# Kernel optimization log

Hardware: AMD Instinct MI355X
Metric: run time of the kernel (lower is better)

The kernel has to match this reference:

```python
import jax, jax.numpy as jnp
import numpy as np

BUCKET_BINS = np.array([0, 1, 2, 3, 4, 5, 7, 8, 15, 16, 31, 32, 63, 64], dtype=np.int32)
MAX_WINDOW = 8  # args.span_maximum_length


def _span_index_table(L):
    # Static enumeration of all spans of width 1..MAX_WINDOW (stride-1 unfold).
    starts, ends = [], []
    for w in range(1, min(L, MAX_WINDOW) + 1):
        s = np.arange(0, L - w + 1)
        starts.append(s)
        ends.append(s + w)
    return (np.concatenate(starts).astype(np.int32),
            np.concatenate(ends).astype(np.int32))


def _bucket(width):
    # index of last bin with width >= bin value
    return jnp.searchsorted(jnp.asarray(BUCKET_BINS), width, side='right') - 1


def _fnn(h, W1, b1, W2, b2, W3, b3):
    # Linear->ReLU->(Dropout: eval identity)->Linear->ReLU->Linear->Softmax
    h = jax.nn.relu(h @ W1 + b1)
    h = jax.nn.relu(h @ W2 + b2)
    return jax.nn.softmax(h @ W3 + b3, axis=-1)


def setup_inputs() -> dict:
    key = jax.random.key(0)
    ks = jax.random.split(key, 16)
    B, L, D = 8, 256, 768
    H, WD, DD = 1024, 25, 25
    span_dim = 2 * D + WD          # 1561
    pair_dim = 2 * span_dim + DD   # 3147
    f = jnp.float32

    def g(k, shape, scale):
        return jax.random.normal(k, shape, dtype=f) * scale

    return {
        'x': g(ks[0], (B, L, D), 1.0),
        'width_emb': g(ks[1], (len(BUCKET_BINS), WD), 0.02),
        'dist_emb': g(ks[2], (len(BUCKET_BINS), DD), 0.02),
        'Ws1': g(ks[3], (span_dim, H), 0.02), 'bs1': jnp.zeros((H,), f),
        'Ws2': g(ks[4], (H, H), 0.02), 'bs2': jnp.zeros((H,), f),
        'Ws3': g(ks[5], (H, 3), 0.02), 'bs3': jnp.zeros((3,), f),
        'Wp1': g(ks[6], (pair_dim, H), 0.02), 'bp1': jnp.zeros((H,), f),
        'Wp2': g(ks[7], (H, H), 0.02), 'bp2': jnp.zeros((H,), f),
        'Wp3': g(ks[8], (H, 4), 0.02), 'bp3': jnp.zeros((4,), f),
        'nz': 64,
    }


def reference(x, width_emb, dist_emb, Ws1, bs1, Ws2, bs2, Ws3, bs3,
              Wp1, bp1, Wp2, bp2, Wp3, bp3, nz):
    B, L, D = x.shape
    starts_np, ends_np = _span_index_table(L)
    starts = jnp.asarray(starts_np)
    ends = jnp.asarray(ends_np)

    # ---- SpanRepresentation: [start token, end token, width bucket emb] ----
    w_emb = width_emb[_bucket(ends - starts)]                     # [S, WD]
    spans = jnp.concatenate([
        x[:, starts_np, :],                                       # [B,S,D]
        x[:, ends_np - 1, :],                                     # [B,S,D]
        jnp.broadcast_to(w_emb, (B,) + w_emb.shape),              # [B,S,WD]
    ], axis=-1)                                                   # [B,S,span_dim]

    # ---- span_fnn + PrunedTargetOpinion (top-k on aspect/opinion probs) ----
    span_prob = _fnn(spans, Ws1, bs1, Ws2, bs2, Ws3, bs3)         # [B,S,3]
    _, t_idx = jax.lax.top_k(span_prob[:, :, 1], nz)              # aspect  [B,nz]
    _, o_idx = jax.lax.top_k(span_prob[:, :, 2], nz)              # opinion [B,nz]

    # ---- PairRepresentation: all target x opinion pairs ----
    t_rep = jnp.take_along_axis(spans, t_idx[:, :, None], axis=1) # [B,nz,sd]
    o_rep = jnp.take_along_axis(spans, o_idx[:, :, None], axis=1)
    ta, tb = starts[t_idx], ends[t_idx]                           # [B,nz]
    oc, od = starts[o_idx], ends[o_idx]
    # min_distance(a,b,c,d) = min(|b-c|, |a-d|)
    dist = jnp.minimum(jnp.abs(tb[:, :, None] - oc[:, None, :]),
                       jnp.abs(ta[:, :, None] - od[:, None, :]))  # [B,nz,nz]
    d_emb = dist_emb[_bucket(dist)]                               # [B,nz,nz,DD]
    sd = spans.shape[-1]
    pairs = jnp.concatenate([
        jnp.broadcast_to(t_rep[:, :, None, :], (B, nz, nz, sd)),
        jnp.broadcast_to(o_rep[:, None, :, :], (B, nz, nz, sd)),
        d_emb,
    ], axis=-1).reshape(B, nz * nz, 2 * sd + d_emb.shape[-1])     # [B,nz^2,pair_dim]

    pair_prob = _fnn(pairs, Wp1, bp1, Wp2, bp2, Wp3, bp3)         # [B,nz^2,4]
    return span_prob, pair_prob
```

## Files before the change

kernel.cpp:

```cpp
#include <hip/hip_runtime.h>
#include <cstdint>
#include <cstddef>

#define BATCH 8
#define SEQ   256
#define DIM   768
#define NSPAN 2020
#define HID   1024
#define NZ    64

typedef unsigned short u16;
typedef unsigned int   u32;
typedef unsigned long long u64;

typedef __bf16 bf16x8 __attribute__((ext_vector_type(8)));
typedef float  f32x4  __attribute__((ext_vector_type(4)));

__device__ __forceinline__ u16 f2bf(float f) {
    union { float f; u32 u; } x; x.f = f;
    u32 r = x.u + 0x7fffu + ((x.u >> 16) & 1u);
    return (u16)(r >> 16);
}
__device__ __forceinline__ float bf2f(u16 b) {
    union { u32 u; float f; } x; x.u = ((u32)b) << 16;
    return x.f;
}
__device__ __forceinline__ void splitbf(float v, u16& h, u16& l) {
    h = f2bf(v);
    l = f2bf(v - bf2f(h));
}

__device__ __forceinline__ void gld_lds16(const void* g, void* l) {
    __builtin_amdgcn_global_load_lds(
        (const __attribute__((address_space(1))) unsigned int*)g,
        (__attribute__((address_space(3))) unsigned int*)l, 16, 0, 0);
}

__device__ __forceinline__ void span_decode(int s, int& start, int& end, int& w) {
    int off = 0;
#pragma unroll
    for (int wi = 1; wi <= 8; ++wi) {
        int cnt = SEQ - wi + 1;
        if (s < off + cnt) { w = wi; start = s - off; end = start + wi; return; }
        off += cnt;
    }
    w = 8; start = 0; end = 8;
}

__device__ __forceinline__ int dbucket(int d) {
    int b = 0;
    b += (d >= 1);  b += (d >= 2);  b += (d >= 3);  b += (d >= 4);
    b += (d >= 5);  b += (d >= 7);  b += (d >= 8);  b += (d >= 15);
    b += (d >= 16); b += (d >= 31); b += (d >= 32); b += (d >= 63);
    b += (d >= 64);
    return b;
}

__device__ __forceinline__ void xcd_map(int L, int sft, int& bx, int& by) {
    int grp = L >> (3 + sft);
    int rem = L & ((1 << (3 + sft)) - 1);
    bx = rem >> 3;
    by = (grp << 3) | (rem & 7);
}

__global__ __launch_bounds__(256) void k_prep(
    const float* __restrict__ x,  u16* __restrict__ xh,   u16* __restrict__ xl,
    const float* __restrict__ wemb, const float* __restrict__ demb,
    const float* __restrict__ bs1, const float* __restrict__ bp1,
    float* __restrict__ wtabS, float* __restrict__ wtabPt,
    float* __restrict__ wtabPo, float* __restrict__ dtab,
    const float* __restrict__ Ws1, u16* __restrict__ W1Th, u16* __restrict__ W1Tl,
    const float* __restrict__ Ws2, u16* __restrict__ W2Th, u16* __restrict__ W2Tl,
    const float* __restrict__ Wp2, u16* __restrict__ Wp2T,
    const float* __restrict__ Wp1, u16* __restrict__ Wp1T4)
{
    __shared__ float tile[32][33];
    const int bid = blockIdx.x, tid = threadIdx.x;
    if (bid < 6144) {
        int i = bid * 256 + tid;
        u16 h, l; splitbf(x[i], h, l);
        xh[i] = h; xl[i] = l;
        return;
    }
    if (bid < 6296) {
        int t = bid - 6144;
        int row = t >> 2;
        int h = (t & 3) * 256 + tid;
        const int wb[8] = {1,2,3,4,5,5,6,7};
        if (row < 8) {
            int bk = wb[row];
            float acc = bs1[h];
            for (int j = 0; j < 25; ++j) acc = fmaf(wemb[bk*25+j], Ws1[(size_t)(1536+j)*HID + h], acc);
            wtabS[row*HID + h] = acc;
        } else if (row < 16) {
            int bk = wb[row-8];
            float acc = 0.f;
            for (int j = 0; j < 25; ++j) acc = fmaf(wemb[bk*25+j], Wp1[(size_t)(1536+j)*HID + h], acc);
            wtabPt[(row-8)*HID + h] = acc;
        } else if (row < 24) {
            int bk = wb[row-16];
            float acc = 0.f;
            for (int j = 0; j < 25; ++j) acc = fmaf(wemb[bk*25+j], Wp1[(size_t)(3097+j)*HID + h], acc);
            wtabPo[(row-16)*HID + h] = acc;
        } else {
            int tt = row - 24;
            float acc = bp1[h];
            for (int j = 0; j < 25; ++j) acc = fmaf(demb[tt*25+j], Wp1[(size_t)(3122+j)*HID + h], acc);
            dtab[tt*HID + h] = acc;
        }
        return;
    }
    const int tb = bid - 6296;
    const int tr = tid >> 3;
    const int tc4 = (tid & 7) * 4;
    int job, tk, tn, blk = 0;
    if (tb < 1536)      { job = 0; tk = tb % 24; tn = tb / 24; }
    else if (tb < 2560) { job = 1; int t = tb - 1536; tk = t & 31; tn = t >> 5; }
    else if (tb < 3584) { job = 2; int t = tb - 2560; tk = t & 31; tn = t >> 5; }
    else                { job = 3; int t = tb - 3584; blk = t / 768; int r = t - blk * 768; tk = r % 24; tn = r / 24; }
    const int k0 = tk * 32, n0 = tn * 32;

    int k = k0 + tr;
    float4 v;
    if (job == 0) {
        const float* s = (n0 < 1024) ? (Ws1 + (size_t)k * HID + n0)
                                     : (Ws1 + (size_t)(768 + k) * HID + (n0 - 1024));
        v = *(const float4*)(s + tc4);
    } else if (job == 1) {
        v = *(const float4*)(Ws2 + (size_t)k * HID + n0 + tc4);
    } else if (job == 2) {
        v = *(const float4*)(Wp2 + (size_t)k * HID + n0 + tc4);
    } else {
        const int roff[4] = {0, 768, 1561, 2329};
        v = *(const float4*)(Wp1 + (size_t)(roff[blk] + k) * HID + n0 + tc4);
    }
    tile[tr][tc4+0] = v.x; tile[tr][tc4+1] = v.y;
    tile[tr][tc4+2] = v.z; tile[tr][tc4+3] = v.w;
    __syncthreads();

    int nn = n0 + tr;
    float w0 = tile[tc4+0][tr], w1 = tile[tc4+1][tr];
    float w2 = tile[tc4+2][tr], w3 = tile[tc4+3][tr];
    if (job == 0) {
        size_t d = (size_t)nn * 768 + k0 + tc4;
        u16 h0,l0,h1,l1,h2,l2,h3,l3;
        splitbf(w0,h0,l0); splitbf(w1,h1,l1); splitbf(w2,h2,l2); splitbf(w3,h3,l3);
        *(uint2*)(W1Th + d) = make_uint2((u32)h0 | ((u32)h1 << 16), (u32)h2 | ((u32)h3 << 16));
        *(uint2*)(W1Tl + d) = make_uint2((u32)l0 | ((u32)l1 << 16), (u32)l2 | ((u32)l3 << 16));
    } else if (job == 1) {
        size_t d = (size_t)nn * 1024 + k0 + tc4;
        u16 h0,l0,h1,l1,h2,l2,h3,l3;
        splitbf(w0,h0,l0); splitbf(w1,h1,l1); splitbf(w2,h2,l2); splitbf(w3,h3,l3);
        *(uint2*)(W2Th + d) = make_uint2((u32)h0 | ((u32)h1 << 16), (u32)h2 | ((u32)h3 << 16));
        *(uint2*)(W2Tl + d) = make_uint2((u32)l0 | ((u32)l1 << 16), (u32)l2 | ((u32)l3 << 16));
    } else if (job == 2) {
        size_t d = (size_t)nn * 1024 + k0 + tc4;
        *(uint2*)(Wp2T + d) = make_uint2((u32)f2bf(w0) | ((u32)f2bf(w1) << 16),
                                         (u32)f2bf(w2) | ((u32)f2bf(w3) << 16));
    } else {
        size_t d = (size_t)blk * 786432 + (size_t)nn * 768 + k0 + tc4;
        *(uint2*)(Wp1T4 + d) = make_uint2((u32)f2bf(w0) | ((u32)f2bf(w1) << 16),
                                          (u32)f2bf(w2) | ((u32)f2bf(w3) << 16));
    }
}

__global__ __launch_bounds__(256) void k_gemm3bf(
    const u16* __restrict__ Ah, const u16* __restrict__ Al, int lda,
    const u16* __restrict__ BTh, const u16* __restrict__ BTl, int ldb,
    float* __restrict__ C, int ldc,
    int M, int K, int nby, int sft)
{
    int bx, by;
    xcd_map(blockIdx.x, sft, bx, by);
    if (by >= nby) return;
    __shared__ __align__(16) u16 sm[4 * 128 * 32];
    u16* sAh = sm;
    u16* sAl = sm + 4096;
    u16* sBh = sm + 8192;
    u16* sBl = sm + 12288;
    const int tid = threadIdx.x;
    const int bm = by * 128, bn = bx * 128;
    const int wave = tid >> 6, lane = tid & 63;
    const int wr = wave >> 1, wc = wave & 1;
    const int q = lane >> 4, tl = lane & 15;

    f32x4 zero = {0.f, 0.f, 0.f, 0.f};
    f32x4 acc[4][4];
#pragma unroll
    for (int i = 0; i < 4; ++i)
#pragma unroll
        for (int j = 0; j < 4; ++j) acc[i][j] = zero;

    const int srow = lane >> 2;
    const int scol = (lane & 3) * 8;
    int ra0 = bm + wave * 32 + srow;      if (ra0 >= M) ra0 = M - 1;
    int ra1 = bm + wave * 32 + 16 + srow; if (ra1 >= M) ra1 = M - 1;
    const int rb0 = bn + wave * 32 + srow;
    const int rb1 = bn + wave * 32 + 16 + srow;
    u16* dA0 = sAh + wave * 1024;  u16* dA1 = dA0 + 512;
    u16* dL0 = sAl + wave * 1024;  u16* dL1 = dL0 + 512;
    u16* dB0 = sBh + wave * 1024;  u16* dB1 = dB0 + 512;
    u16* dC0 = sBl + wave * 1024;  u16* dC1 = dC0 + 512;
    const u16* gA0 = Ah  + (size_t)ra0 * lda + scol;
    const u16* gA1 = Ah  + (size_t)ra1 * lda + scol;
    const u16* gL0 = Al  + (size_t)ra0 * lda + scol;
    const u16* gL1 = Al  + (size_t)ra1 * lda + scol;
    const u16* gB0 = BTh + (size_t)rb0 * ldb + scol;
    const u16* gB1 = BTh + (size_t)rb1 * ldb + scol;
    const u16* gC0 = BTl + (size_t)rb0 * ldb + scol;
    const u16* gC1 = BTl + (size_t)rb1 * ldb + scol;

    for (int k0 = 0; k0 < K; k0 += 32) {
        gld_lds16(gA0 + k0, dA0);
        gld_lds16(gA1 + k0, dA1);
        gld_lds16(gL0 + k0, dL0);
        gld_lds16(gL1 + k0, dL1);
        gld_lds16(gB0 + k0, dB0);
        gld_lds16(gB1 + k0, dB1);
        gld_lds16(gC0 + k0, dC0);
        gld_lds16(gC1 + k0, dC1);
        __syncthreads();
        bf16x8 ah[4], al[4], bh[4], bl[4];
#pragma unroll
        for (int t = 0; t < 4; ++t) {
            int arow = (wr*64 + t*16 + tl) * 32 + q*8;
            int brow = (wc*64 + t*16 + tl) * 32 + q*8;
            ah[t] = *(const bf16x8*)(&sAh[arow]);
            al[t] = *(const bf16x8*)(&sAl[arow]);
            bh[t] = *(const bf16x8*)(&sBh[brow]);
            bl[t] = *(const bf16x8*)(&sBl[brow]);
        }
#pragma unroll
        for (int ti = 0; ti < 4; ++ti)
#pragma unroll
            for (int tj = 0; tj < 4; ++tj) {
                acc[ti][tj] = __builtin_amdgcn_mfma_f32_16x16x32_bf16(ah[ti], bh[tj], acc[ti][tj], 0, 0, 0);
                acc[ti][tj] = __builtin_amdgcn_mfma_f32_16x16x32_bf16(al[ti], bh[tj], acc[ti][tj], 0, 0, 0);
                acc[ti][tj] = __builtin_amdgcn_mfma_f32_16x16x32_bf16(ah[ti], bl[tj], acc[ti][tj], 0, 0, 0);
            }
        __syncthreads();
    }
#pragma unroll
    for (int ti = 0; ti < 4; ++ti) {
#pragma unroll
        for (int tj = 0; tj < 4; ++tj) {
            int gcol = bn + wc*64 + tj*16 + tl;
#pragma unroll
            for (int r = 0; r < 4; ++r) {
                int grow = bm + wr*64 + ti*16 + q*4 + r;
                if (grow >= M) continue;
                C[(size_t)grow * ldc + gcol] = acc[ti][tj][r];
            }
        }
    }
}

#define MFB __builtin_amdgcn_mfma_f32_16x16x32_bf16
#define MFROW(i, A, B) \
    acc[i][0] = MFB(A, B[0], acc[i][0], 0, 0, 0); \
    acc[i][1] = MFB(A, B[1], acc[i][1], 0, 0, 0); \
    acc[i][2] = MFB(A, B[2], acc[i][2], 0, 0, 0); \
    acc[i][3] = MFB(A, B[3], acc[i][3], 0, 0, 0);

#define SPAN_PHASE(P, VMC, GLDS) \
    { \
        bf16x8 ah0 = *(const bf16x8*)(smr + rA + (2*(P)+0)*512); \
        bf16x8 ah1 = *(const bf16x8*)(smr + rA + (2*(P)+1)*512); \
        bf16x8 al0 = *(const bf16x8*)(smr + rA + 8192 + (2*(P)+0)*512); \
        bf16x8 al1 = *(const bf16x8*)(smr + rA + 8192 + (2*(P)+1)*512); \
        if ((P) == 0) { \
            bh[0] = *(const bf16x8*)(smr + rB + 0*512); \
            bh[1] = *(const bf16x8*)(smr + rB + 1*512); \
            bh[2] = *(const bf16x8*)(smr + rB + 2*512); \
            bh[3] = *(const bf16x8*)(smr + rB + 3*512); \
            bl[0] = *(const bf16x8*)(smr + rB + 8192 + 0*512); \
            bl[1] = *(const bf16x8*)(smr + rB + 8192 + 1*512); \
            bl[2] = *(const bf16x8*)(smr + rB + 8192 + 2*512); \
            bl[3] = *(const bf16x8*)(smr + rB + 8192 + 3*512); \
        } \
        GLDS \
        asm volatile("s_waitcnt vmcnt(" #VMC ")" ::: "memory"); \
        asm volatile("s_barrier" ::: "memory"); \
        __builtin_amdgcn_sched_barrier(0); \
        __builtin_amdgcn_s_setprio(1); \
        MFROW(2*(P)+0, ah0, bh) \
        MFROW(2*(P)+1, ah1, bh) \
        MFROW(2*(P)+0, al0, bh) \
        MFROW(2*(P)+1, al1, bh) \
        MFROW(2*(P)+0, ah0, bl) \
        MFROW(2*(P)+1, ah1, bl) \
        __builtin_amdgcn_s_setprio(0); \
        asm volatile("s_barrier" ::: "memory"); \
    }

__global__ __launch_bounds__(512, 2) void k_span_l2(
    const u16* __restrict__ Ah, const u16* __restrict__ Al,
    const u16* __restrict__ BTh, const u16* __restrict__ BTl,
    const float* __restrict__ bs2, const float* __restrict__ Ws3,
    float* __restrict__ part, int M)
{
    __shared__ __align__(16) u16 sm[65536];
    const int tid = threadIdx.x;
    const int swz = (blockIdx.x & 7) * 32 + (blockIdx.x >> 3);
    const int by = swz >> 2, bx = swz & 3;
    const int bm = by * 256, bn = bx * 256;
    const int wave = tid >> 6, lane = tid & 63;
    const int wm = wave >> 2, wn = wave & 3;
    const int tl = lane & 15, q8 = lane >> 4;

    const int sr  = lane >> 2;
    const int scs = lane & 3;
    const int scl = scs ^ ((sr >> 1) & 3);
    const u16* gsrc[8];
    u32 ldst[8];
#pragma unroll
    for (int c = 0; c < 4; ++c) {
        int arr  = 2 + (c >> 1);
        int half = c & 1;
        int sb   = wave;
        int row  = bn + half * 128 + sb * 16 + sr;
        const u16* base = (arr == 2) ? BTh : BTl;
        gsrc[c] = base + (size_t)row * HID + scl * 8;
        ldst[c] = arr * 8192 + half * 4096 + sb * 512;
    }
#pragma unroll
    for (int p = 0; p < 4; ++p) {
        int arr  = wave >> 2;
        int half = (wave >> 1) & 1;
        int sb   = 2 * p + (wave & 1);
        int row  = bm + half * 128 + sb * 16 + sr;
        if (row >= M) row = M - 1;
        const u16* base = arr ? Al : Ah;
        gsrc[4 + p] = base + (size_t)row * HID + scl * 8;
        ldst[4 + p] = arr * 8192 + half * 4096 + sb * 512;
    }
    const int cpr = q8 ^ ((tl >> 1) & 3);
    const u32 lof = (u32)(tl * 32 + cpr * 8);
    const u32 rA  = (u32)(wm * 4096) + lof;
    const u32 rB  = 16384u + (u32)((wn >> 1) * 4096 + (wn & 1) * 2048) + lof;

    f32x4 zero = {0.f, 0.f, 0.f, 0.f};
    f32x4 acc[8][4];
#pragma unroll
    for (int i = 0; i < 8; ++i)
#pragma unroll
        for (int j = 0; j < 4; ++j) acc[i][j] = zero;

#pragma unroll
    for (int c = 0; c < 8; ++c) gld_lds16(gsrc[c], sm + ldst[c]);
    asm volatile("s_waitcnt vmcnt(3)" ::: "memory");
    asm volatile("s_barrier" ::: "memory");

    bf16x8 bh[4], bl[4];
    for (int t = 0; t < 32; ++t) {
        const u16* smr = sm + ((t & 1) ? 32768u : 0u);
        u16*       smw = sm + ((t & 1) ? 0u : 32768u);
        const int  kn  = (t + 1) * 32;
        SPAN_PHASE(0, 5,
            gld_lds16(gsrc[0] + kn, smw + ldst[0]);
            gld_lds16(gsrc[1] + kn, smw + ldst[1]);
            gld_lds16(gsrc[2] + kn, smw + ldst[2]);)
        SPAN_PHASE(1, 6,
            gld_lds16(gsrc[3] + kn, smw + ldst[3]);
            gld_lds16(gsrc[4] + kn, smw + ldst[4]);)
        SPAN_PHASE(2, 7,
            gld_lds16(gsrc[5] + kn, smw + ldst[5]);
            gld_lds16(gsrc[6] + kn, smw + ldst[6]);)
        SPAN_PHASE(3, 3,
            gld_lds16(gsrc[7] + kn, smw + ldst[7]);)
    }

    const int slot = bx * 4 + wn;
#pragma unroll
    for (int fm = 0; fm < 8; ++fm) {
#pragma unroll
        for (int r = 0; r < 4; ++r) {
            int grow = bm + wm * 128 + fm * 16 + q8 * 4 + r;
            float l0 = 0.f, l1 = 0.f, l2 = 0.f;
#pragma unroll
            for (int fn = 0; fn < 4; ++fn) {
                int gcol = bn + wn * 64 + fn * 16 + tl;
                float v = fmaxf(acc[fm][fn][r] + bs2[gcol], 0.f);
                const float* w3 = Ws3 + gcol * 3;
                l0 = fmaf(v, w3[0], l0);
                l1 = fmaf(v, w3[1], l1);
                l2 = fmaf(v, w3[2], l2);
            }
#pragma unroll
            for (int off = 8; off > 0; off >>= 1) {
                l0 += __shfl_down(l0, off, 16);
                l1 += __shfl_down(l1, off, 16);
                l2 += __shfl_down(l2, off, 16);
            }
            if (tl == 0 && grow < M) {
                float* dst = part + ((size_t)grow * 16 + slot) * 3;
                dst[0] = l0; dst[1] = l1; dst[2] = l2;
            }
        }
    }
    asm volatile("s_waitcnt vmcnt(0)" ::: "memory");
}

__global__ __launch_bounds__(256) void k_pairL1(
    const u16* __restrict__ xh, const u16* __restrict__ Wp1T4,
    float* __restrict__ TO2, const int* __restrict__ toks)
{
    __shared__ __align__(16) u16 sm[2 * 64 * 32];
    u16* sA = sm;
    u16* sB = sm + 2048;
    const int tid = threadIdx.x;
    const int bid = blockIdx.x;
    const int p = bid >> 8;
    const int bx = bid & 15, by = (bid >> 4) & 15;
    const int bm = by * 64, bn = bx * 64;
    const int wave = tid >> 6, lane = tid & 63;
    const int wr = wave >> 1, wc = wave & 1;
    const int q = lane >> 4, tl = lane & 15;
    const bool isO = bm >= 512;

    f32x4 zero = {0.f, 0.f, 0.f, 0.f};
    f32x4 acc[2][2];
#pragma unroll
    for (int i = 0; i < 2; ++i)
#pragma unroll
        for (int j = 0; j < 2; ++j) acc[i][j] = zero;

    const int srow = tid >> 2;
    const int scol = (tid & 3) * 8;
    u16* dA = sA + wave * 512;
    u16* dB = sB + wave * 512;

    int arow = toks[bm + srow + p * 1024];
    const u16* gA = xh + (size_t)arow * DIM + scol;
    const u16* gB = Wp1T4 + ((size_t)((isO ? 2 : 0) + p) * 1024 + bn + srow) * DIM + scol;
    for (int k0 = 0; k0 < DIM; k0 += 32) {
        gld_lds16(gA + k0, dA);
        gld_lds16(gB + k0, dB);
        __syncthreads();
        bf16x8 af[2], bf[2];
#pragma unroll
        for (int t = 0; t < 2; ++t) {
            af[t] = *(const bf16x8*)(&sA[(wr*32 + t*16 + tl) * 32 + q*8]);
            bf[t] = *(const bf16x8*)(&sB[(wc*32 + t*16 + tl) * 32 + q*8]);
        }
#pragma unroll
        for (int ti = 0; ti < 2; ++ti)
#pragma unroll
            for (int tj = 0; tj < 2; ++tj)
                acc[ti][tj] = __builtin_amdgcn_mfma_f32_16x16x32_bf16(af[ti], bf[tj], acc[ti][tj], 0, 0, 0);
        __syncthreads();
    }
    float* dstb = TO2 + (size_t)p * 1024 * HID;
#pragma unroll
    for (int ti = 0; ti < 2; ++ti) {
#pragma unroll
        for (int tj = 0; tj < 2; ++tj) {
            int gcol = bn + wc*32 + tj*16 + tl;
#pragma unroll
            for (int r = 0; r < 4; ++r) {
                int grow = bm + wr*32 + ti*16 + q*4 + r;
                dstb[(size_t)grow * HID + gcol] = acc[ti][tj][r];
            }
        }
    }
}

__global__ __launch_bounds__(256) void k_build_h1s(
    const float* __restrict__ XALL, const float* __restrict__ wtabS,
    u16* __restrict__ h1h, u16* __restrict__ h1l)
{
    int r = blockIdx.x;
    int b = r / NSPAN, s = r - b * NSPAN;
    int st, en, w; span_decode(s, st, en, w);
    const float4* xs = (const float4*)(XALL + (size_t)(b*SEQ + st) * 2048);
    const float4* xe = (const float4*)(XALL + (size_t)(b*SEQ + en - 1) * 2048 + 1024);
    const float4* wt = (const float4*)(wtabS + (size_t)(w-1) * HID);
    int t = threadIdx.x;
    float4 a = xs[t], bz = xe[t], c = wt[t];
    float v0 = fmaxf(a.x + bz.x + c.x, 0.f);
    float v1 = fmaxf(a.y + bz.y + c.y, 0.f);
    float v2 = fmaxf(a.z + bz.z + c.z, 0.f);
    float v3 = fmaxf(a.w + bz.w + c.w, 0.f);
    u16 h0,l0,h1,l1,h2,l2,h3,l3;
    splitbf(v0,h0,l0); splitbf(v1,h1,l1); splitbf(v2,h2,l2); splitbf(v3,h3,l3);
    size_t base = (size_t)r * HID + t * 4;
    *(uint2*)(h1h + base) = make_uint2((u32)h0 | ((u32)h1 << 16), (u32)h2 | ((u32)h3 << 16));
    *(uint2*)(h1l + base) = make_uint2((u32)l0 | ((u32)l1 << 16), (u32)l2 | ((u32)l3 << 16));
}

__global__ __launch_bounds__(1024) void k_topk(
    const float* __restrict__ partS, const float* __restrict__ bs3,
    float* __restrict__ out, int* __restrict__ t_idx, int* __restrict__ o_idx,
    int* __restrict__ toks)
{
    int b = blockIdx.x >> 1;
    int head = 1 + (blockIdx.x & 1);
    int* outp = (head == 1 ? t_idx : o_idx) + b * NZ;
    __shared__ u64 keys[2048];
    int tid = threadIdx.x;
#pragma unroll
    for (int ii = 0; ii < 2; ++ii) {
        int s = tid + ii * 1024;
        u32 fb = 0;
        if (s < NSPAN) {
            const float* p = partS + (size_t)(b * NSPAN + s) * 48;
            float s0 = bs3[0], s1 = bs3[1], s2 = bs3[2];
#pragma unroll
            for (int t = 0; t < 16; ++t) {
                s0 += p[t*3]; s1 += p[t*3+1]; s2 += p[t*3+2];
            }
            float m = fmaxf(s0, fmaxf(s1, s2));
            float e0 = expf(s0 - m), e1 = expf(s1 - m), e2 = expf(s2 - m);
            float inv = 1.f / (e0 + e1 + e2);
            float p0 = e0 * inv, p1 = e1 * inv, p2 = e2 * inv;
            float* o = out + (size_t)(b * NSPAN + s) * 3;
            o[0] = p0; o[1] = p1; o[2] = p2;
            union { float f; u32 u; } x;
            x.f = (head == 1) ? p1 : p2;
            fb = x.u;
        }
        keys[s] = ((u64)fb << 32) | (u64)(0xFFFFFFFFu - (u32)s);
    }
    __syncthreads();
    for (int k = 2; k <= 2048; k <<= 1) {
        for (int j = k >> 1; j > 0; j >>= 1) {
#pragma unroll
            for (int ii = 0; ii < 2; ++ii) {
                int i = tid + ii * 1024;
                int ixj = i ^ j;
                if (ixj > i) {
                    u64 a = keys[i], c = keys[ixj];
                    bool desc = (i & k) == 0;
                    bool wrong = desc ? (a < c) : (a > c);
                    if (wrong) { keys[i] = c; keys[ixj] = a; }
                }
            }
            __syncthreads();
        }
    }
    if (tid < NZ) {
        u64 key = keys[tid];
        int fi = (int)(0xFFFFFFFFu - (u32)(key & 0xFFFFFFFFu));
        if (fi < 0 || fi >= NSPAN) fi = 0;
        outp[tid] = fi;
        int st, en, w; span_decode(fi, st, en, w);
        int base = (head == 1 ? 0 : 512) + b * NZ + tid;
        toks[base] = b * SEQ + st;
        toks[1024 + base] = b * SEQ + en - 1;
    }
}

__global__ __launch_bounds__(256) void k_build_h1p(
    const float* __restrict__ TO2, const int* __restrict__ t_idx, const int* __restrict__ o_idx,
    const float* __restrict__ wtabPt, const float* __restrict__ wtabPo,
    const float* __restrict__ dtab, u16* __restrict__ h1p)
{
    __shared__ float Ts[8][HID];
    __shared__ float Os[4][HID];
    const int bid = blockIdx.x;
    const int b = bid >> 7;
    const int it = (bid >> 4) & 7;
    const int jt = bid & 15;
    const int i0 = it * 8, j0 = jt * 4;
    const int tid = threadIdx.x;
    const int k4 = tid * 4;
    const size_t PS = (size_t)1024 * HID;

    int tinfo[8][2];
    int oinfo[4][2];
#pragma unroll
    for (int r = 0; r < 8; ++r) {
        int i = i0 + r;
        int ts = t_idx[b*64 + i];
        int ta, tb, wt; span_decode(ts, ta, tb, wt);
        tinfo[r][0] = ta; tinfo[r][1] = tb;
        float4 t0 = *(const float4*)(TO2 + (size_t)(b*64 + i) * HID + k4);
        float4 t1 = *(const float4*)(TO2 + PS + (size_t)(b*64 + i) * HID + k4);
        float4 pp = *(const float4*)(wtabPt + (size_t)(wt-1) * HID + k4);
        Ts[r][k4+0] = t0.x + t1.x + pp.x;
        Ts[r][k4+1] = t0.y + t1.y + pp.y;
        Ts[r][k4+2] = t0.z + t1.z + pp.z;
        Ts[r][k4+3] = t0.w + t1.w + pp.w;
    }
#pragma unroll
    for (int r = 0; r < 4; ++r) {
        int j = j0 + r;
        int os = o_idx[b*64 + j];
        int oc, od, wo; span_decode(os, oc, od, wo);
        oinfo[r][0] = oc; oinfo[r][1] = od;
        float4 o0 = *(const float4*)(TO2 + (size_t)(512 + b*64 + j) * HID + k4);
        float4 o1 = *(const float4*)(TO2 + PS + (size_t)(512 + b*64 + j) * HID + k4);
        float4 qq = *(const float4*)(wtabPo + (size_t)(wo-1) * HID + k4);
        Os[r][k4+0] = o0.x + o1.x + qq.x;
        Os[r][k4+1] = o0.y + o1.y + qq.y;
        Os[r][k4+2] = o0.z + o1.z + qq.z;
        Os[r][k4+3] = o0.w + o1.w + qq.w;
    }
    __syncthreads();

#pragma unroll
    for (int ri = 0; ri < 8; ++ri) {
#pragma unroll
        for (int rj = 0; rj < 4; ++rj) {
            int ta = tinfo[ri][0], tb = tinfo[ri][1];
            int oc = oinfo[rj][0], od = oinfo[rj][1];
            int d1 = tb - oc; d1 = d1 < 0 ? -d1 : d1;
            int d2 = ta - od; d2 = d2 < 0 ? -d2 : d2;
            int dist = d1 < d2 ? d1 : d2;
            int db = dbucket(dist);
            const float4 dd = *(const float4*)(dtab + (size_t)db * HID + k4);
            float vx = fmaxf(Ts[ri][k4+0] + Os[rj][k4+0] + dd.x, 0.f);
            float vy = fmaxf(Ts[ri][k4+1] + Os[rj][k4+1] + dd.y, 0.f);
            float vz = fmaxf(Ts[ri][k4+2] + Os[rj][k4+2] + dd.z, 0.f);
            float vw = fmaxf(Ts[ri][k4+3] + Os[rj][k4+3] + dd.w, 0.f);
            u32 p0 = (u32)f2bf(vx) | ((u32)f2bf(vy) << 16);
            u32 p1 = (u32)f2bf(vz) | ((u32)f2bf(vw) << 16);
            int row = b * 4096 + (i0 + ri) * 64 + (j0 + rj);
            *(uint2*)(h1p + (size_t)row * HID + k4) = make_uint2(p0, p1);
        }
    }
}

#define PAIR_PHASE(P, VMC, GLDS) \
    { \
        bf16x8 a00 = *(const bf16x8*)(smr + rA + ((2*(P)+0)*2+0)*512); \
        bf16x8 a01 = *(const bf16x8*)(smr + rA + ((2*(P)+0)*2+1)*512); \
        bf16x8 a10 = *(const bf16x8*)(smr + rA + ((2*(P)+1)*2+0)*512); \
        bf16x8 a11 = *(const bf16x8*)(smr + rA + ((2*(P)+1)*2+1)*512); \
        if ((P) == 0) { \
            b0[0] = *(const bf16x8*)(smr + rB + 0*512); \
            b1[0] = *(const bf16x8*)(smr + rB + 1*512); \
            b0[1] = *(const bf16x8*)(smr + rB + 2*512); \
            b1[1] = *(const bf16x8*)(smr + rB + 3*512); \
            b0[2] = *(const bf16x8*)(smr + rB + 4*512); \
            b1[2] = *(const bf16x8*)(smr + rB + 5*512); \
            b0[3] = *(const bf16x8*)(smr + rB + 6*512); \
            b1[3] = *(const bf16x8*)(smr + rB + 7*512); \
        } \
        GLDS \
        asm volatile("s_waitcnt vmcnt(" #VMC ")" ::: "memory"); \
        asm volatile("s_barrier" ::: "memory"); \
        __builtin_amdgcn_sched_barrier(0); \
        __builtin_amdgcn_s_setprio(1); \
        MFROW(2*(P)+0, a00, b0) \
        MFROW(2*(P)+1, a10, b0) \
        MFROW(2*(P)+0, a01, b1) \
        MFROW(2*(P)+1, a11, b1) \
        __builtin_amdgcn_s_setprio(0); \
        asm volatile("s_barrier" ::: "memory"); \
    }

__global__ __launch_bounds__(512, 2) void k_pair_l2(
    const u16* __restrict__ Abf, const u16* __restrict__ BT,
    const float* __restrict__ bp2, const float* __restrict__ Wp3,
    float* __restrict__ part)
{
    __shared__ __align__(16) u16 sm[65536];
    const int tid = threadIdx.x;
    const int swz = (blockIdx.x & 7) * 64 + (blockIdx.x >> 3);
    const int by = swz >> 2, bx = swz & 3;
    const int bm = by * 256, bn = bx * 256;
    const int wave = tid >> 6, lane = tid & 63;
    const int wm = wave >> 2, wn = wave & 3;
    const int tl = lane & 15, q8 = lane >> 4;

    const int sr  = lane >> 2;
    const int scs = lane & 3;
    const int scl = scs ^ ((sr >> 1) & 3);
    const u16* gsrc[8];
    u32 ldst[8];
#pragma unroll
    for (int c = 0; c < 4; ++c) {
        int half = c >> 1;
        int sb   = (c & 1) * 8 + wave;
        int row  = bn + half * 128 + (sb >> 1) * 16 + sr;
        gsrc[c] = BT + (size_t)row * HID + (sb & 1) * 32 + scl * 8;
        ldst[c] = 16384 + half * 8192 + sb * 512;
    }
#pragma unroll
    for (int p = 0; p < 4; ++p) {
        int half = wave >> 2;
        int sb   = 4 * p + (wave & 3);
        int row  = bm + half * 128 + (sb >> 1) * 16 + sr;
        gsrc[4 + p] = Abf + (size_t)row * HID + (sb & 1) * 32 + scl * 8;
        ldst[4 + p] = half * 8192 + sb * 512;
    }
    const int cpr = q8 ^ ((tl >> 1) & 3);
    const u32 lof = (u32)(tl * 32 + cpr * 8);
    const u32 rA  = (u32)(wm * 8192) + lof;
    const u32 rB  = 16384u + (u32)((wn >> 1) * 8192 + (wn & 1) * 4096) + lof;

    f32x4 zero = {0.f, 0.f, 0.f, 0.f};
    f32x4 acc[8][4];
#pragma unroll
    for (int i = 0; i < 8; ++i)
#pragma unroll
        for (int j = 0; j < 4; ++j) acc[i][j] = zero;

#pragma unroll
    for (int c = 0; c < 8; ++c) gld_lds16(gsrc[c], sm + ldst[c]);
    asm volatile("s_waitcnt vmcnt(3)" ::: "memory");
    asm volatile("s_barrier" ::: "memory");

    bf16x8 b0[4], b1[4];
    for (int t = 0; t < 16; ++t) {
        const u16* smr = sm + ((t & 1) ? 32768u : 0u);
        u16*       smw = sm + ((t & 1) ? 0u : 32768u);
        const int  kn  = (t + 1) * 64;
        PAIR_PHASE(0, 5,
            gld_lds16(gsrc[0] + kn, smw + ldst[0]);
            gld_lds16(gsrc[1] + kn, smw + ldst[1]);
            gld_lds16(gsrc[2] + kn, smw + ldst[2]);)
        PAIR_PHASE(1, 6,
            gld_lds16(gsrc[3] + kn, smw + ldst[3]);
            gld_lds16(gsrc[4] + kn, smw + ldst[4]);)
        PAIR_PHASE(2, 7,
            gld_lds16(gsrc[5] + kn, smw + ldst[5]);
            gld_lds16(gsrc[6] + kn, smw + ldst[6]);)
        PAIR_PHASE(3, 3,
            gld_lds16(gsrc[7] + kn, smw + ldst[7]);)
    }

    const int slot = bx * 4 + wn;
#pragma unroll
    for (int fm = 0; fm < 8; ++fm) {
#pragma unroll
        for (int r = 0; r < 4; ++r) {
            int grow = bm + wm * 128 + fm * 16 + q8 * 4 + r;
            float l0 = 0.f, l1 = 0.f, l2 = 0.f, l3 = 0.f;
#pragma unroll
            for (int fn = 0; fn < 4; ++fn) {
                int gcol = bn + wn * 64 + fn * 16 + tl;
                float v = fmaxf(acc[fm][fn][r] + bp2[gcol], 0.f);
                const float4 w = *(const float4*)(Wp3 + gcol * 4);
                l0 = fmaf(v, w.x, l0); l1 = fmaf(v, w.y, l1);
                l2 = fmaf(v, w.z, l2); l3 = fmaf(v, w.w, l3);
            }
#pragma unroll
            for (int off = 8; off > 0; off >>= 1) {
                l0 += __shfl_down(l0, off, 16);
                l1 += __shfl_down(l1, off, 16);
                l2 += __shfl_down(l2, off, 16);
                l3 += __shfl_down(l3, off, 16);
            }
            if (tl == 0) {
                float* dst = part + ((size_t)grow * 16 + slot) * 4;
                dst[0] = l0; dst[1] = l1; dst[2] = l2; dst[3] = l3;
            }
        }
    }
    asm volatile("s_waitcnt vmcnt(0)" ::: "memory");
}

__global__ __launch_bounds__(256) void k_pair_red(
    const float* __restrict__ part, const float* __restrict__ bp3,
    float* __restrict__ out)
{
    int r = blockIdx.x * 256 + threadIdx.x;
    const float4* p = (const float4*)(part + (size_t)r * 64);
    float s0 = bp3[0], s1 = bp3[1], s2 = bp3[2], s3 = bp3[3];
#pragma unroll
    for (int t = 0; t < 16; ++t) {
        float4 v = p[t];
        s0 += v.x; s1 += v.y; s2 += v.z; s3 += v.w;
    }
    float m = fmaxf(fmaxf(s0, s1), fmaxf(s2, s3));
    float e0 = expf(s0 - m), e1 = expf(s1 - m), e2 = expf(s2 - m), e3 = expf(s3 - m);
    float inv = 1.f / (e0 + e1 + e2 + e3);
    float* o = out + (size_t)r * 4;
    o[0] = e0 * inv; o[1] = e1 * inv; o[2] = e2 * inv; o[3] = e3 * inv;
}

extern "C" void kernel_launch(void* const* d_in, const int* in_sizes, int n_in,
                              void* d_out, int out_size, void* d_ws, size_t ws_size,
                              hipStream_t stream)
{
    const float* x    = (const float*)d_in[0];
    const float* wemb = (const float*)d_in[1];
    const float* demb = (const float*)d_in[2];
    const float* Ws1  = (const float*)d_in[3];
    const float* bs1  = (const float*)d_in[4];
    const float* Ws2  = (const float*)d_in[5];
    const float* bs2  = (const float*)d_in[6];
    const float* Ws3  = (const float*)d_in[7];
    const float* bs3  = (const float*)d_in[8];
    const float* Wp1  = (const float*)d_in[9];
    const float* bp1  = (const float*)d_in[10];
    const float* Wp2  = (const float*)d_in[11];
    const float* bp2  = (const float*)d_in[12];
    const float* Wp3  = (const float*)d_in[13];
    const float* bp3  = (const float*)d_in[14];
    float* out = (float*)d_out;
    char* ws = (char*)d_ws;

    const size_t RSZ = (size_t)32768 * HID * 2;
    size_t off = 0;
    auto alloc = [&](size_t bytes) -> void* {
        void* p = ws + off;
        off += (bytes + 255) & ~(size_t)255;
        return p;
    };
    char* R1 = (char*)alloc(RSZ);
    char* R2 = (char*)alloc(RSZ);
    u16*   h1h  = (u16*)R1;
    u16*   h1l  = (u16*)(R1 + (size_t)16160 * HID * 2);
    float* XALL = (float*)R2;
    u16*   xl   = (u16*)(R2 + (16u << 20));
    u16*   W1Th = (u16*)(R2 + (19u << 20));
    u16*   W1Tl = (u16*)(R2 + (22u << 20));
    u16*   h1p  = (u16*)R2;
    u16*   xh     = (u16*)alloc((size_t)2048 * DIM * 2);
    float* TO2    = (float*)alloc((size_t)2 * 1024 * HID * 4);
    float* partS  = (float*)alloc((size_t)16160 * 16 * 3 * 4);
    float* partP  = (float*)alloc((size_t)32768 * 16 * 4 * 4);
    u16*   W2Th   = (u16*)alloc((size_t)1024 * 1024 * 2);
    u16*   W2Tl   = (u16*)alloc((size_t)1024 * 1024 * 2);
    u16*   Wp2T   = (u16*)alloc((size_t)1024 * 1024 * 2);
    u16*   Wp1T4  = (u16*)alloc((size_t)4 * 1024 * 768 * 2);
    float* wtabS  = (float*)alloc(8 * HID * 4);
    float* wtabPt = (float*)alloc(8 * HID * 4);
    float* wtabPo = (float*)alloc(8 * HID * 4);
    float* dtab   = (float*)alloc(14 * HID * 4);
    int*   t_idx  = (int*)alloc(BATCH * NZ * 4);
    int*   o_idx  = (int*)alloc(BATCH * NZ * 4);
    int*   toks   = (int*)alloc(2048 * 4);
    (void)ws_size; (void)in_sizes; (void)n_in; (void)out_size;

    k_prep<<<12952, 256, 0, stream>>>(x, xh, xl, wemb, demb, bs1, bp1,
                                      wtabS, wtabPt, wtabPo, dtab,
                                      Ws1, W1Th, W1Tl, Ws2, W2Th, W2Tl,
                                      Wp2, Wp2T, Wp1, Wp1T4);

    k_gemm3bf<<<256, 256, 0, stream>>>(xh, xl, 768, W1Th, W1Tl, 768,
                                       XALL, 2048, 2048, 768, 16, 4);
    k_build_h1s<<<16160, 256, 0, stream>>>(XALL, wtabS, h1h, h1l);
    k_span_l2<<<256, 512, 0, stream>>>(h1h, h1l, W2Th, W2Tl, bs2, Ws3, partS, 16160);
    k_topk<<<16, 1024, 0, stream>>>(partS, bs3, out, t_idx, o_idx, toks);
    k_pairL1<<<512, 256, 0, stream>>>(xh, Wp1T4, TO2, toks);
    k_build_h1p<<<1024, 256, 0, stream>>>(TO2, t_idx, o_idx, wtabPt, wtabPo, dtab, h1p);
    k_pair_l2<<<512, 512, 0, stream>>>(h1p, Wp2T, bp2, Wp3, partP);
    k_pair_red<<<128, 256, 0, stream>>>(partP, bp3, out + 48480);
}
```

Baseline: 410.5 us.

## Software-pipeline LDS fragment reads into registers in span and pair GEMM loops

Restructures the main K loops of the span and pair layer-2 GEMM kernels. The A fragments for the next phase are double-buffered in two register sets (X/Y), and the B fragments for the next tile are loaded at the end of each iteration. This lets the LDS reads overlap the MFMA work of the current phase and drops the trailing barrier after each phase. The risk is that the end-of-iteration reads from the write buffer may run before all async global-to-LDS copies have landed, since only vmcnt(3) is waited on. The change also raises register pressure.

New measurement: 410.5 us. No clear change (-0.0%).

```diff
diff --git a/kernel.cpp b/kernel.cpp
--- a/kernel.cpp
+++ b/kernel.cpp
@@ -262,37 +262,6 @@
     acc[i][2] = MFB(A, B[2], acc[i][2], 0, 0, 0); \
     acc[i][3] = MFB(A, B[3], acc[i][3], 0, 0, 0);
 
-#define SPAN_PHASE(P, VMC, GLDS) \
-    { \
-        bf16x8 ah0 = *(const bf16x8*)(smr + rA + (2*(P)+0)*512); \
-        bf16x8 ah1 = *(const bf16x8*)(smr + rA + (2*(P)+1)*512); \
-        bf16x8 al0 = *(const bf16x8*)(smr + rA + 8192 + (2*(P)+0)*512); \
-        bf16x8 al1 = *(const bf16x8*)(smr + rA + 8192 + (2*(P)+1)*512); \
-        if ((P) == 0) { \
-            bh[0] = *(const bf16x8*)(smr + rB + 0*512); \
-            bh[1] = *(const bf16x8*)(smr + rB + 1*512); \
-            bh[2] = *(const bf16x8*)(smr + rB + 2*512); \
-            bh[3] = *(const bf16x8*)(smr + rB + 3*512); \
-            bl[0] = *(const bf16x8*)(smr + rB + 8192 + 0*512); \
-            bl[1] = *(const bf16x8*)(smr + rB + 8192 + 1*512); \
-            bl[2] = *(const bf16x8*)(smr + rB + 8192 + 2*512); \
-            bl[3] = *(const bf16x8*)(smr + rB + 8192 + 3*512); \
-        } \
-        GLDS \
-        asm volatile("s_waitcnt vmcnt(" #VMC ")" ::: "memory"); \
-        asm volatile("s_barrier" ::: "memory"); \
-        __builtin_amdgcn_sched_barrier(0); \
-        __builtin_amdgcn_s_setprio(1); \
-        MFROW(2*(P)+0, ah0, bh) \
-        MFROW(2*(P)+1, ah1, bh) \
-        MFROW(2*(P)+0, al0, bh) \
-        MFROW(2*(P)+1, al1, bh) \
-        MFROW(2*(P)+0, ah0, bl) \
-        MFROW(2*(P)+1, ah1, bl) \
-        __builtin_amdgcn_s_setprio(0); \
-        asm volatile("s_barrier" ::: "memory"); \
-    }
-
 __global__ __launch_bounds__(512, 2) void k_span_l2(
     const u16* __restrict__ Ah, const u16* __restrict__ Al,
     const u16* __restrict__ BTh, const u16* __restrict__ BTl,
@@ -352,22 +321,87 @@
     asm volatile("s_barrier" ::: "memory");
 
     bf16x8 bh[4], bl[4];
+    bf16x8 aXh0, aXh1, aXl0, aXl1, aYh0, aYh1, aYl0, aYl1;
+#pragma unroll
+    for (int fn = 0; fn < 4; ++fn) {
+        bh[fn] = *(const bf16x8*)(sm + rB + fn * 512);
+        bl[fn] = *(const bf16x8*)(sm + rB + 8192 + fn * 512);
+    }
+    aXh0 = *(const bf16x8*)(sm + rA + 0 * 512);
+    aXh1 = *(const bf16x8*)(sm + rA + 1 * 512);
+    aXl0 = *(const bf16x8*)(sm + rA + 8192 + 0 * 512);
+    aXl1 = *(const bf16x8*)(sm + rA + 8192 + 1 * 512);
+
     for (int t = 0; t < 32; ++t) {
         const u16* smr = sm + ((t & 1) ? 32768u : 0u);
         u16*       smw = sm + ((t & 1) ? 0u : 32768u);
         const int  kn  = (t + 1) * 32;
-        SPAN_PHASE(0, 5,
-            gld_lds16(gsrc[0] + kn, smw + ldst[0]);
-            gld_lds16(gsrc[1] + kn, smw + ldst[1]);
-            gld_lds16(gsrc[2] + kn, smw + ldst[2]);)
-        SPAN_PHASE(1, 6,
-            gld_lds16(gsrc[3] + kn, smw + ldst[3]);
-            gld_lds16(gsrc[4] + kn, smw + ldst[4]);)
-        SPAN_PHASE(2, 7,
-            gld_lds16(gsrc[5] + kn, smw + ldst[5]);
-            gld_lds16(gsrc[6] + kn, smw + ldst[6]);)
-        SPAN_PHASE(3, 3,
-            gld_lds16(gsrc[7] + kn, smw + ldst[7]);)
+        gld_lds16(gsrc[0] + kn, smw + ldst[0]);
+        gld_lds16(gsrc[1] + kn, smw + ldst[1]);
+        gld_lds16(gsrc[2] + kn, smw + ldst[2]);
+        asm volatile("s_waitcnt vmcnt(5)" ::: "memory");
+        asm volatile("s_barrier" ::: "memory");
+        __builtin_amdgcn_sched_barrier(0);
+        __builtin_amdgcn_s_setprio(1);
+        MFROW(0, aXh0, bh) MFROW(1, aXh1, bh)
+        MFROW(0, aXl0, bh) MFROW(1, aXl1, bh)
+        MFROW(0, aXh0, bl) MFROW(1, aXh1, bl)
+        __builtin_amdgcn_s_setprio(0);
+        __builtin_amdgcn_sched_barrier(0);
+        aYh0 = *(const bf16x8*)(smr + rA + 2 * 512);
+        aYh1 = *(const bf16x8*)(smr + rA + 3 * 512);
+        aYl0 = *(const bf16x8*)(smr + rA + 8192 + 2 * 512);
+        aYl1 = *(const bf16x8*)(smr + rA + 8192 + 3 * 512);
+        gld_lds16(gsrc[3] + kn, smw + ldst[3]);
+        gld_lds16(gsrc[4] + kn, smw + ldst[4]);
+        asm volatile("s_waitcnt vmcnt(6)" ::: "memory");
+        asm volatile("s_barrier" ::: "memory");
+        __builtin_amdgcn_sched_barrier(0);
+        __builtin_amdgcn_s_setprio(1);
+        MFROW(2, aYh0, bh) MFROW(3, aYh1, bh)
+        MFROW(2, aYl0, bh) MFROW(3, aYl1, bh)
+        MFROW(2, aYh0, bl) MFROW(3, aYh1, bl)
+        __builtin_amdgcn_s_setprio(0);
+        __builtin_amdgcn_sched_barrier(0);
+        aXh0 = *(const bf16x8*)(smr + rA + 4 * 512);
+        aXh1 = *(const bf16x8*)(smr + rA + 5 * 512);
+        aXl0 = *(const bf16x8*)(smr + rA + 8192 + 4 * 512);
+        aXl1 = *(const bf16x8*)(smr + rA + 8192 + 5 * 512);
+        gld_lds16(gsrc[5] + kn, smw + ldst[5]);
+        gld_lds16(gsrc[6] + kn, smw + ldst[6]);
+        asm volatile("s_waitcnt vmcnt(7)" ::: "memory");
+        asm volatile("s_barrier" ::: "memory");
+        __builtin_amdgcn_sched_barrier(0);
+        __builtin_amdgcn_s_setprio(1);
+        MFROW(4, aXh0, bh) MFROW(5, aXh1, bh)
+        MFROW(4, aXl0, bh) MFROW(5, aXl1, bh)
+        MFROW(4, aXh0, bl) MFROW(5, aXh1, bl)
+        __builtin_amdgcn_s_setprio(0);
+        __builtin_amdgcn_sched_barrier(0);
+        aYh0 = *(const bf16x8*)(smr + rA + 6 * 512);
+        aYh1 = *(const bf16x8*)(smr + rA + 7 * 512);
+        aYl0 = *(const bf16x8*)(smr + rA + 8192 + 6 * 512);
+        aYl1 = *(const bf16x8*)(smr + rA + 8192 + 7 * 512);
+        gld_lds16(gsrc[7] + kn, smw + ldst[7]);
+        asm volatile("s_waitcnt vmcnt(3)" ::: "memory");
+        asm volatile("s_barrier" ::: "memory");
+        __builtin_amdgcn_sched_barrier(0);
+        __builtin_amdgcn_s_setprio(1);
+        MFROW(6, aYh0, bh) MFROW(7, aYh1, bh)
+        MFROW(6, aYl0, bh) MFROW(7, aYl1, bh)
+        MFROW(6, aYh0, bl) MFROW(7, aYh1, bl)
+        __builtin_amdgcn_s_setprio(0);
+        __builtin_amdgcn_sched_barrier(0);
+        aXh0 = *(const bf16x8*)(smw + rA + 0 * 512);
+        aXh1 = *(const bf16x8*)(smw + rA + 1 * 512);
+        aXl0 = *(const bf16x8*)(smw + rA + 8192 + 0 * 512);
+        aXl1 = *(const bf16x8*)(smw + rA + 8192 + 1 * 512);
+#pragma unroll
+        for (int fn = 0; fn < 4; ++fn) {
+            bh[fn] = *(const bf16x8*)(smw + rB + fn * 512);
+            bl[fn] = *(const bf16x8*)(smw + rB + 8192 + fn * 512);
+        }
+        asm volatile("s_barrier" ::: "memory");
     }
 
     const int slot = bx * 4 + wn;
@@ -621,34 +655,11 @@
     }
 }
 
-#define PAIR_PHASE(P, VMC, GLDS) \
-    { \
-        bf16x8 a00 = *(const bf16x8*)(smr + rA + ((2*(P)+0)*2+0)*512); \
-        bf16x8 a01 = *(const bf16x8*)(smr + rA + ((2*(P)+0)*2+1)*512); \
-        bf16x8 a10 = *(const bf16x8*)(smr + rA + ((2*(P)+1)*2+0)*512); \
-        bf16x8 a11 = *(const bf16x8*)(smr + rA + ((2*(P)+1)*2+1)*512); \
-        if ((P) == 0) { \
-            b0[0] = *(const bf16x8*)(smr + rB + 0*512); \
-            b1[0] = *(const bf16x8*)(smr + rB + 1*512); \
-            b0[1] = *(const bf16x8*)(smr + rB + 2*512); \
-            b1[1] = *(const bf16x8*)(smr + rB + 3*512); \
-            b0[2] = *(const bf16x8*)(smr + rB + 4*512); \
-            b1[2] = *(const bf16x8*)(smr + rB + 5*512); \
-            b0[3] = *(const bf16x8*)(smr + rB + 6*512); \
-            b1[3] = *(const bf16x8*)(smr + rB + 7*512); \
-        } \
-        GLDS \
-        asm volatile("s_waitcnt vmcnt(" #VMC ")" ::: "memory"); \
-        asm volatile("s_barrier" ::: "memory"); \
-        __builtin_amdgcn_sched_barrier(0); \
-        __builtin_amdgcn_s_setprio(1); \
-        MFROW(2*(P)+0, a00, b0) \
-        MFROW(2*(P)+1, a10, b0) \
-        MFROW(2*(P)+0, a01, b1) \
-        MFROW(2*(P)+1, a11, b1) \
-        __builtin_amdgcn_s_setprio(0); \
-        asm volatile("s_barrier" ::: "memory"); \
-    }
+#define MFROWP(i, A0, A1, B0, B1) \
+    acc[i][0] = MFB(A0, B0[0], acc[i][0], 0, 0, 0); \
+    acc[i][1] = MFB(A0, B0[1], acc[i][1], 0, 0, 0); \
+    acc[i][2] = MFB(A0, B0[2], acc[i][2], 0, 0, 0); \
+    acc[i][3] = MFB(A0, B0[3], acc[i][3], 0, 0, 0);
 
 __global__ __launch_bounds__(512, 2) void k_pair_l2(
     const u16* __restrict__ Abf, const u16* __restrict__ BT,
@@ -703,22 +714,83 @@
     asm volatile("s_barrier" ::: "memory");
 
     bf16x8 b0[4], b1[4];
+    bf16x8 xa00, xa01, xa10, xa11, ya00, ya01, ya10, ya11;
+#pragma unroll
+    for (int fn = 0; fn < 4; ++fn) {
+        b0[fn] = *(const bf16x8*)(sm + rB + (fn * 2 + 0) * 512);
+        b1[fn] = *(const bf16x8*)(sm + rB + (fn * 2 + 1) * 512);
+    }
+    xa00 = *(const bf16x8*)(sm + rA + 0 * 512);
+    xa01 = *(const bf16x8*)(sm + rA + 1 * 512);
+    xa10 = *(const bf16x8*)(sm + rA + 2 * 512);
+    xa11 = *(const bf16x8*)(sm + rA + 3 * 512);
+
     for (int t = 0; t < 16; ++t) {
         const u16* smr = sm + ((t & 1) ? 32768u : 0u);
         u16*       smw = sm + ((t & 1) ? 0u : 32768u);
         const int  kn  = (t + 1) * 64;
-        PAIR_PHASE(0, 5,
-            gld_lds16(gsrc[0] + kn, smw + ldst[0]);
-            gld_lds16(gsrc[1] + kn, smw + ldst[1]);
-            gld_lds16(gsrc[2] + kn, smw + ldst[2]);)
-        PAIR_PHASE(1, 6,
-            gld_lds16(gsrc[3] + kn, smw + ldst[3]);
-            gld_lds16(gsrc[4] + kn, smw + ldst[4]);)
-        PAIR_PHASE(2, 7,
-            gld_lds16(gsrc[5] + kn, smw + ldst[5]);
-            gld_lds16(gsrc[6] + kn, smw + ldst[6]);)
-        PAIR_PHASE(3, 3,
-            gld_lds16(gsrc[7] + kn, smw + ldst[7]);)
+        gld_lds16(gsrc[0] + kn, smw + ldst[0]);
+        gld_lds16(gsrc[1] + kn, smw + ldst[1]);
+        gld_lds16(gsrc[2] + kn, smw + ldst[2]);
+        asm volatile("s_waitcnt vmcnt(5)" ::: "memory");
+        asm volatile("s_barrier" ::: "memory");
+        __builtin_amdgcn_sched_barrier(0);
+        __builtin_amdgcn_s_setprio(1);
+        MFROW(0, xa00, b0) MFROW(1, xa10, b0)
+        MFROW(0, xa01, b1) MFROW(1, xa11, b1)
+        __builtin_amdgcn_s_setprio(0);
+        __builtin_amdgcn_sched_barrier(0);
+        ya00 = *(const bf16x8*)(smr + rA + 4 * 512);
+        ya01 = *(const bf16x8*)(smr + rA + 5 * 512);
+        ya10 = *(const bf16x8*)(smr + rA + 6 * 512);
+        ya11 = *(const bf16x8*)(smr + rA + 7 * 512);
+        gld_lds16(gsrc[3] + kn, smw + ldst[3]);
+        gld_lds16(gsrc[4] + kn, smw + ldst[4]);
+        asm volatile("s_waitcnt vmcnt(6)" ::: "memory");
+        asm volatile("s_barrier" ::: "memory");
+        __builtin_amdgcn_sched_barrier(0);
+        __builtin_amdgcn_s_setprio(1);
+        MFROW(2, ya00, b0) MFROW(3, ya10, b0)
+        MFROW(2, ya01, b1) MFROW(3, ya11, b1)
+        __builtin_amdgcn_s_setprio(0);
+        __builtin_amdgcn_sched_barrier(0);
+        xa00 = *(const bf16x8*)(smr + rA + 8 * 512);
+        xa01 = *(const bf16x8*)(smr + rA + 9 * 512);
+        xa10 = *(const bf16x8*)(smr + rA + 10 * 512);
+        xa11 = *(const bf16x8*)(smr + rA + 11 * 512);
+        gld_lds16(gsrc[5] + kn, smw + ldst[5]);
+        gld_lds16(gsrc[6] + kn, smw + ldst[6]);
+        asm volatile("s_waitcnt vmcnt(7)" ::: "memory");
+        asm volatile("s_barrier" ::: "memory");
+        __builtin_amdgcn_sched_barrier(0);
+        __builtin_amdgcn_s_setprio(1);
+        MFROW(4, xa00, b0) MFROW(5, xa10, b0)
+        MFROW(4, xa01, b1) MFROW(5, xa11, b1)
+        __builtin_amdgcn_s_setprio(0);
+        __builtin_amdgcn_sched_barrier(0);
+        ya00 = *(const bf16x8*)(smr + rA + 12 * 512);
+        ya01 = *(const bf16x8*)(smr + rA + 13 * 512);
+        ya10 = *(const bf16x8*)(smr + rA + 14 * 512);
+        ya11 = *(const bf16x8*)(smr + rA + 15 * 512);
+        gld_lds16(gsrc[7] + kn, smw + ldst[7]);
+        asm volatile("s_waitcnt vmcnt(3)" ::: "memory");
+        asm volatile("s_barrier" ::: "memory");
+        __builtin_amdgcn_sched_barrier(0);
+        __builtin_amdgcn_s_setprio(1);
+        MFROW(6, ya00, b0) MFROW(7, ya10, b0)
+        MFROW(6, ya01, b1) MFROW(7, ya11, b1)
+        __builtin_amdgcn_s_setprio(0);
+        __builtin_amdgcn_sched_barrier(0);
+        xa00 = *(const bf16x8*)(smw + rA + 0 * 512);
+        xa01 = *(const bf16x8*)(smw + rA + 1 * 512);
+        xa10 = *(const bf16x8*)(smw + rA + 2 * 512);
+        xa11 = *(const bf16x8*)(smw + rA + 3 * 512);
+#pragma unroll
+        for (int fn = 0; fn < 4; ++fn) {
+            b0[fn] = *(const bf16x8*)(smw + rB + (fn * 2 + 0) * 512);
+            b1[fn] = *(const bf16x8*)(smw + rB + (fn * 2 + 1) * 512);
+        }
+        asm volatile("s_barrier" ::: "memory");
     }
 
     const int slot = bx * 4 + wn;
```
